# Kernel optimization log

Measured on AMD Instinct MI355X. Metric: run time of the kernel, lower is better.

## Reference

```python
import jax, jax.numpy as jnp
import numpy as np

D_TOK = 64
HID = 128


def _init_linear(key, fan_in, fan_out, bias_fill=None):
    kw, kb = jax.random.split(key)
    bound = 1.0 / np.sqrt(fan_in)
    W = jax.random.uniform(kw, (fan_in, fan_out), jnp.float32, -bound, bound)
    if bias_fill is None:
        b = jax.random.uniform(kb, (fan_out,), jnp.float32, -bound, bound)
    else:
        b = jnp.full((fan_out,), bias_fill, jnp.float32)
    return W, b


def setup_inputs() -> dict:
    key = jax.random.key(0)
    ks = jax.random.split(key, 7)
    N, E = 20000, 16
    tokens = jax.random.normal(ks[0], (N, E, D_TOK), jnp.float32)
    enc_W1, enc_b1 = _init_linear(ks[1], D_TOK, HID)
    enc_W2, enc_b2 = _init_linear(ks[2], HID, HID)
    spec_W1, spec_b1 = _init_linear(ks[3], 4 * HID, HID)
    spec_W2, spec_b2 = _init_linear(ks[4], HID, 1)
    def_W1, def_b1 = _init_linear(ks[5], 3 * HID, HID)
    def_W2, def_b2 = _init_linear(ks[6], HID, 1, bias_fill=-1.0)  # config.defer_bias
    return {
        "tokens": tokens,
        "enc_W1": enc_W1, "enc_b1": enc_b1, "enc_W2": enc_W2, "enc_b2": enc_b2,
        "spec_W1": spec_W1, "spec_b1": spec_b1, "spec_W2": spec_W2, "spec_b2": spec_b2,
        "def_W1": def_W1, "def_b1": def_b1, "def_W2": def_W2, "def_b2": def_b2,
        "full_index": 0,
        "top_k": 2,
    }


def _apply_top_k_mask(logits, full_index, top_k):
    # logits: [N, E]; mimic torch _apply_top_k_mask
    N, E = logits.shape
    if E <= 1:
        return logits
    neg = jnp.finfo(logits.dtype).min
    k = max(1, min(int(top_k), E - 1))
    masked = logits.at[:, full_index].set(neg)
    _, idx = jax.lax.top_k(masked, k)  # [N, k]
    rows = jnp.arange(N)[:, None]
    keep = jnp.zeros((N, E), bool).at[rows, idx].set(True)
    keep = keep.at[:, full_index].set(False)
    return jnp.where(keep, masked, neg)


def reference(tokens, enc_W1, enc_b1, enc_W2, enc_b2,
              spec_W1, spec_b1, spec_W2, spec_b2,
              def_W1, def_b1, def_W2, def_b2,
              full_index, top_k):
    neg = jnp.finfo(tokens.dtype).min
    # token encoder: two Linear+ReLU, applied per (row, expert)
    h = jax.nn.relu(tokens @ enc_W1 + enc_b1)
    encoded = jax.nn.relu(h @ enc_W2 + enc_b2)          # [N, E, H]
    full_token = encoded[:, full_index:full_index + 1]  # [N, 1, H]
    global_token = encoded.mean(axis=1, keepdims=True)  # [N, 1, H]
    token_delta = encoded - full_token
    global_delta = encoded - global_token
    pair = jnp.concatenate([encoded, token_delta, global_delta,
                            jnp.abs(token_delta)], axis=-1)  # [N, E, 4H]
    spec_h = jax.nn.relu(pair @ spec_W1 + spec_b1)
    specialist_logits = (spec_h @ spec_W2 + spec_b2)[..., 0]  # [N, E]
    specialist_logits = specialist_logits.at[:, full_index].set(neg)
    sparse_logits = _apply_top_k_mask(specialist_logits, full_index, top_k)
    w = jax.nn.softmax(sparse_logits, axis=1)
    w = w.at[:, full_index].set(0.0)
    mass = w.sum(axis=1, keepdims=True)
    w = jnp.where(mass > 0, w / jnp.maximum(mass, 1e-8), jnp.zeros_like(w))
    pooled = jnp.concatenate([full_token[:, 0], global_token[:, 0],
                              jnp.abs(token_delta).mean(axis=1)], axis=1)  # [N, 3H]
    def_h = jax.nn.relu(pooled @ def_W1 + def_b1)
    defer_prob = jax.nn.sigmoid(def_h @ def_W2 + def_b2)  # [N, 1]
    return w, defer_prob
```

## Files before the change

### kernel.cpp

```cpp
#include <hip/hip_runtime.h>
#include <math.h>

#define E 16
#define D 64
#define H 128
#define R 4
#define ROWS (R * E)
#define MW 16

__global__ void wabc_prep(const float* __restrict__ specW1, float* __restrict__ wabc) {
    int i = blockIdx.x * blockDim.x + threadIdx.x;
    if (i < H * H) {
        wabc[i] = specW1[i] + specW1[H * H + i] + specW1[2 * H * H + i];
    }
}

template <bool USE_WABC>
__global__ __launch_bounds__(256, 2)
void router_kernel(const float* __restrict__ tokens,
                   const float* __restrict__ encW1, const float* __restrict__ encB1,
                   const float* __restrict__ encW2, const float* __restrict__ encB2,
                   const float* __restrict__ specW1, const float* __restrict__ specB1,
                   const float* __restrict__ specW2,
                   const float* __restrict__ defW1, const float* __restrict__ defB1,
                   const float* __restrict__ defW2, const float* __restrict__ defB2,
                   const int* __restrict__ fiPtr, const int* __restrict__ tkPtr,
                   const float* __restrict__ wabc,
                   float* __restrict__ out, int N) {
    __shared__ float bufA[ROWS * H];
    __shared__ float bufB[ROWS * H];
    __shared__ float s_full[R * H];
    __shared__ float s_glob[R * H];
    __shared__ float s_mabs[R * H];
    __shared__ float s_bias[R * H];
    __shared__ float s_logits[ROWS];
    __shared__ float s_dred[R];

    const int tid   = threadIdx.x;
    const int n0    = blockIdx.x * R;
    const int fi    = fiPtr[0];
    const int lane  = tid & 63;
    const int wq    = tid >> 6;
    const int mbase = wq * MW;
    const int hw    = lane >> 5;
    const int jl    = lane & 31;
    const int jw0   = jl * 4;
    const int mb2   = mbase + hw * 8;

    {
        const size_t base  = (size_t)n0 * (E * D);
        const size_t total = (size_t)N * (E * D);
        float4* dst = (float4*)bufA;
#pragma unroll
        for (int it = 0; it < 4; it++) {
            int f = tid + it * 256;
            size_t off = base + (size_t)f * 4;
            float4 v = make_float4(0.f, 0.f, 0.f, 0.f);
            if (off + 3 < total) v = *(const float4*)(tokens + off);
            dst[f] = v;
        }
    }
    __syncthreads();

    {
        float acc[8][4];
#pragma unroll
        for (int m = 0; m < 8; m++)
#pragma unroll
            for (int j = 0; j < 4; j++) acc[m][j] = 0.f;
#pragma unroll 2
        for (int k = 0; k < D; k += 4) {
            float4 w0 = *(const float4*)(encW1 + (k + 0) * H + jw0);
            float4 w1 = *(const float4*)(encW1 + (k + 1) * H + jw0);
            float4 w2 = *(const float4*)(encW1 + (k + 2) * H + jw0);
            float4 w3 = *(const float4*)(encW1 + (k + 3) * H + jw0);
#pragma unroll
            for (int m = 0; m < 8; m++) {
                float4 t = *(const float4*)(bufA + (mb2 + m) * D + k);
                acc[m][0] = fmaf(t.w, w3.x, fmaf(t.z, w2.x, fmaf(t.y, w1.x, fmaf(t.x, w0.x, acc[m][0]))));
                acc[m][1] = fmaf(t.w, w3.y, fmaf(t.z, w2.y, fmaf(t.y, w1.y, fmaf(t.x, w0.y, acc[m][1]))));
                acc[m][2] = fmaf(t.w, w3.z, fmaf(t.z, w2.z, fmaf(t.y, w1.z, fmaf(t.x, w0.z, acc[m][2]))));
                acc[m][3] = fmaf(t.w, w3.w, fmaf(t.z, w2.w, fmaf(t.y, w1.w, fmaf(t.x, w0.w, acc[m][3]))));
            }
        }
        float4 b = *(const float4*)(encB1 + jw0);
#pragma unroll
        for (int m = 0; m < 8; m++) {
            float4 o;
            o.x = fmaxf(acc[m][0] + b.x, 0.f);
            o.y = fmaxf(acc[m][1] + b.y, 0.f);
            o.z = fmaxf(acc[m][2] + b.z, 0.f);
            o.w = fmaxf(acc[m][3] + b.w, 0.f);
            *(float4*)(bufB + (mb2 + m) * H + jw0) = o;
        }
    }
    __syncthreads();

    {
        float acc[8][4];
#pragma unroll
        for (int m = 0; m < 8; m++)
#pragma unroll
            for (int j = 0; j < 4; j++) acc[m][j] = 0.f;
#pragma unroll 2
        for (int k = 0; k < H; k += 4) {
            float4 w0 = *(const float4*)(encW2 + (k + 0) * H + jw0);
            float4 w1 = *(const float4*)(encW2 + (k + 1) * H + jw0);
            float4 w2 = *(const float4*)(encW2 + (k + 2) * H + jw0);
            float4 w3 = *(const float4*)(encW2 + (k + 3) * H + jw0);
#pragma unroll
            for (int m = 0; m < 8; m++) {
                float4 t = *(const float4*)(bufB + (mb2 + m) * H + k);
                acc[m][0] = fmaf(t.w, w3.x, fmaf(t.z, w2.x, fmaf(t.y, w1.x, fmaf(t.x, w0.x, acc[m][0]))));
                acc[m][1] = fmaf(t.w, w3.y, fmaf(t.z, w2.y, fmaf(t.y, w1.y, fmaf(t.x, w0.y, acc[m][1]))));
                acc[m][2] = fmaf(t.w, w3.z, fmaf(t.z, w2.z, fmaf(t.y, w1.z, fmaf(t.x, w0.z, acc[m][2]))));
                acc[m][3] = fmaf(t.w, w3.w, fmaf(t.z, w2.w, fmaf(t.y, w1.w, fmaf(t.x, w0.w, acc[m][3]))));
            }
        }
        float4 b = *(const float4*)(encB2 + jw0);
#pragma unroll
        for (int m = 0; m < 8; m++) {
            float4 o;
            o.x = fmaxf(acc[m][0] + b.x, 0.f);
            o.y = fmaxf(acc[m][1] + b.y, 0.f);
            o.z = fmaxf(acc[m][2] + b.z, 0.f);
            o.w = fmaxf(acc[m][3] + b.w, 0.f);
            *(float4*)(bufA + (mb2 + m) * H + jw0) = o;
        }
    }
    __syncthreads();

    {
        const int r4 = tid >> 6;
        const int cb = tid & 63;
#pragma unroll
        for (int half = 0; half < 2; half++) {
            const int c = cb + half * 64;
            const float* er = bufA + (r4 * E) * H + c;
            float v[E];
#pragma unroll
            for (int e = 0; e < E; e++) v[e] = er[e * H];
            float s = 0.f;
#pragma unroll
            for (int e = 0; e < E; e++) s += v[e];
            float fc = v[fi];
            float ma = 0.f;
#pragma unroll
            for (int e = 0; e < E; e++) ma += fabsf(v[e] - fc);
            s_full[r4 * H + c] = fc;
            s_glob[r4 * H + c] = s * (1.f / 16.f);
            s_mabs[r4 * H + c] = ma * (1.f / 16.f);
        }
    }
    __syncthreads();

    float* s_pB = bufB;
    float* s_pD = bufB + 2 * R * H;
    {
        const int jp = tid & 63;
        const int jj = jp * 2;
        const int kh = (tid >> 6) & 1;
        const int rg = tid >> 7;
        const int c0 = kh * 64;
        const float* __restrict__ Wb = specW1 + H * H;
        const float* __restrict__ Wc = specW1 + 2 * H * H;
        float accB[2][2] = {{0.f, 0.f}, {0.f, 0.f}};
        float accD[2][2] = {{0.f, 0.f}, {0.f, 0.f}};
        for (int cc = 0; cc < 64; cc++) {
            const int c = c0 + cc;
            float2 wb = *(const float2*)(Wb + c * H + jj);
            float2 wc = *(const float2*)(Wc + c * H + jj);
            float2 d0 = *(const float2*)(defW1 + c * H + jj);
            float2 d1 = *(const float2*)(defW1 + (H + c) * H + jj);
            float2 d2 = *(const float2*)(defW1 + (2 * H + c) * H + jj);
#pragma unroll
            for (int rl = 0; rl < 2; rl++) {
                const int r = rg * 2 + rl;
                float fv = s_full[r * H + c];
                float gv = s_glob[r * H + c];
                float mv = s_mabs[r * H + c];
                accB[rl][0] = fmaf(fv, wb.x, accB[rl][0]);
                accB[rl][1] = fmaf(fv, wb.y, accB[rl][1]);
                accB[rl][0] = fmaf(gv, wc.x, accB[rl][0]);
                accB[rl][1] = fmaf(gv, wc.y, accB[rl][1]);
                accD[rl][0] = fmaf(fv, d0.x, accD[rl][0]);
                accD[rl][1] = fmaf(fv, d0.y, accD[rl][1]);
                accD[rl][0] = fmaf(gv, d1.x, accD[rl][0]);
                accD[rl][1] = fmaf(gv, d1.y, accD[rl][1]);
                accD[rl][0] = fmaf(mv, d2.x, accD[rl][0]);
                accD[rl][1] = fmaf(mv, d2.y, accD[rl][1]);
            }
        }
#pragma unroll
        for (int rl = 0; rl < 2; rl++) {
            const int r = rg * 2 + rl;
            *(float2*)(s_pB + (kh * R + r) * H + jj) = make_float2(accB[rl][0], accB[rl][1]);
            *(float2*)(s_pD + (kh * R + r) * H + jj) = make_float2(accD[rl][0], accD[rl][1]);
        }
    }
    __syncthreads();

    {
        float dv = 0.f;
#pragma unroll
        for (int t = 0; t < 2; t++) {
            const int j = lane + t * 64;
            float pb = s_pB[wq * H + j] + s_pB[(R + wq) * H + j];
            s_bias[wq * H + j] = specB1[j] - pb;
            float pd = defB1[j] + s_pD[wq * H + j] + s_pD[(R + wq) * H + j];
            dv += fmaxf(pd, 0.f) * defW2[j];
        }
#pragma unroll
        for (int off = 32; off; off >>= 1) dv += __shfl_xor(dv, off, 64);
        if (lane == 0) s_dred[wq] = dv;
    }
    __syncthreads();

    {
        float acc[8][4];
#pragma unroll
        for (int m = 0; m < 8; m++)
#pragma unroll
            for (int j = 0; j < 4; j++) acc[m][j] = 0.f;
        const float* __restrict__ Wd = specW1 + 3 * H * H;
        for (int k = 0; k < H; k += 4) {
            float4 wa0, wa1, wa2, wa3;
            if (USE_WABC) {
                wa0 = *(const float4*)(wabc + (k + 0) * H + jw0);
                wa1 = *(const float4*)(wabc + (k + 1) * H + jw0);
                wa2 = *(const float4*)(wabc + (k + 2) * H + jw0);
                wa3 = *(const float4*)(wabc + (k + 3) * H + jw0);
            } else {
#pragma unroll
                for (int t = 0; t < 4; t++) {
                    const float* p = specW1 + (k + t) * H + jw0;
                    float4 x0 = *(const float4*)(p);
                    float4 x1 = *(const float4*)(p + H * H);
                    float4 x2 = *(const float4*)(p + 2 * H * H);
                    float4 s4 = make_float4(x0.x + x1.x + x2.x, x0.y + x1.y + x2.y,
                                            x0.z + x1.z + x2.z, x0.w + x1.w + x2.w);
                    if (t == 0) wa0 = s4; else if (t == 1) wa1 = s4;
                    else if (t == 2) wa2 = s4; else wa3 = s4;
                }
            }
            float4 wd0 = *(const float4*)(Wd + (k + 0) * H + jw0);
            float4 wd1 = *(const float4*)(Wd + (k + 1) * H + jw0);
            float4 wd2 = *(const float4*)(Wd + (k + 2) * H + jw0);
            float4 wd3 = *(const float4*)(Wd + (k + 3) * H + jw0);
            float4 f4 = *(const float4*)(s_full + wq * H + k);
#pragma unroll
            for (int m = 0; m < 8; m++) {
                float4 ev = *(const float4*)(bufA + (mb2 + m) * H + k);
                float ax = fabsf(ev.x - f4.x);
                float ay = fabsf(ev.y - f4.y);
                float az = fabsf(ev.z - f4.z);
                float aw = fabsf(ev.w - f4.w);
#pragma unroll
                for (int j = 0; j < 4; j++) {
                    const float* waj0 = &wa0.x, *waj1 = &wa1.x, *waj2 = &wa2.x, *waj3 = &wa3.x;
                    const float* wdj0 = &wd0.x, *wdj1 = &wd1.x, *wdj2 = &wd2.x, *wdj3 = &wd3.x;
                    float a = acc[m][j];
                    a = fmaf(ev.x, waj0[j], a);
                    a = fmaf(ev.y, waj1[j], a);
                    a = fmaf(ev.z, waj2[j], a);
                    a = fmaf(ev.w, waj3[j], a);
                    a = fmaf(ax, wdj0[j], a);
                    a = fmaf(ay, wdj1[j], a);
                    a = fmaf(az, wdj2[j], a);
                    a = fmaf(aw, wdj3[j], a);
                    acc[m][j] = a;
                }
            }
        }
        float4 bn = *(const float4*)(s_bias + wq * H + jw0);
        float4 w2 = *(const float4*)(specW2 + jw0);
#pragma unroll
        for (int m = 0; m < 8; m++) {
            float p = 0.f;
            p += fmaxf(acc[m][0] + bn.x, 0.f) * w2.x;
            p += fmaxf(acc[m][1] + bn.y, 0.f) * w2.y;
            p += fmaxf(acc[m][2] + bn.z, 0.f) * w2.z;
            p += fmaxf(acc[m][3] + bn.w, 0.f) * w2.w;
#pragma unroll
            for (int off = 1; off < 32; off <<= 1) p += __shfl_xor(p, off, 64);
            if (jl == 0) s_logits[mb2 + m] = p;
        }
    }
    __syncthreads();

    if (tid < R && (n0 + tid) < N) {
        const int r = tid;
        const int n = n0 + r;
        float s = s_dred[r] + defB2[0];
        out[(size_t)N * E + n] = 1.f / (1.f + expf(-s));
        int k = tkPtr[0];
        if (k < 1) k = 1;
        if (k > E - 1) k = E - 1;
        unsigned chosen = 0u;
        for (int kk = 0; kk < k; kk++) {
            float bv = -INFINITY;
            int bi = 0;
            for (int e = 0; e < E; e++) {
                if (e == fi || ((chosen >> e) & 1u)) continue;
                float v = s_logits[r * E + e];
                if (v > bv) { bv = v; bi = e; }
            }
            chosen |= (1u << bi);
        }
        float mx = -INFINITY;
        for (int e = 0; e < E; e++)
            if ((chosen >> e) & 1u) { float v = s_logits[r * E + e]; if (v > mx) mx = v; }
        float ssum = 0.f;
        for (int e = 0; e < E; e++)
            if ((chosen >> e) & 1u) ssum += expf(s_logits[r * E + e] - mx);
        float inv = 1.f / ssum;
        for (int e = 0; e < E; e++) {
            float wv = 0.f;
            if ((chosen >> e) & 1u) wv = expf(s_logits[r * E + e] - mx) * inv;
            out[(size_t)n * E + e] = wv;
        }
    }
}

extern "C" void kernel_launch(void* const* d_in, const int* in_sizes, int n_in,
                              void* d_out, int out_size, void* d_ws, size_t ws_size,
                              hipStream_t stream) {
    (void)n_in; (void)out_size;
    const float* tokens = (const float*)d_in[0];
    const float* encW1  = (const float*)d_in[1];
    const float* encB1  = (const float*)d_in[2];
    const float* encW2  = (const float*)d_in[3];
    const float* encB2  = (const float*)d_in[4];
    const float* specW1 = (const float*)d_in[5];
    const float* specB1 = (const float*)d_in[6];
    const float* specW2 = (const float*)d_in[7];
    const float* defW1  = (const float*)d_in[9];
    const float* defB1  = (const float*)d_in[10];
    const float* defW2  = (const float*)d_in[11];
    const float* defB2  = (const float*)d_in[12];
    const int*   fiPtr  = (const int*)d_in[13];
    const int*   tkPtr  = (const int*)d_in[14];
    float* out = (float*)d_out;

    const int N = in_sizes[0] / (E * D);
    const int grid = (N + R - 1) / R;
    const bool useWs = (d_ws != nullptr) && (ws_size >= (size_t)(H * H * sizeof(float)));

    if (useWs) {
        wabc_prep<<<(H * H + 255) / 256, 256, 0, stream>>>(specW1, (float*)d_ws);
        router_kernel<true><<<grid, 256, 0, stream>>>(
            tokens, encW1, encB1, encW2, encB2, specW1, specB1, specW2,
            defW1, defB1, defW2, defB2, fiPtr, tkPtr, (const float*)d_ws, out, N);
    } else {
        router_kernel<false><<<grid, 256, 0, stream>>>(
            tokens, encW1, encB1, encW2, encB2, specW1, specB1, specW2,
            defW1, defB1, defW2, defB2, fiPtr, tkPtr, nullptr, out, N);
    }
}
```

Baseline: 739.5 us.

## Cut LDS footprint by streaming tokens from global and splitting encoder into halves

Tokens are no longer staged in shared memory; the first encoder layer reads them straight from global memory. The encoder runs in two passes of 32 rows each, so the hidden buffer shrinks to 32 rows, and the pooled/bias scratch arrays are aliased into that buffer. Launch bounds go from 2 to 3 blocks per CU to use the freed LDS and raise occupancy. The cost is more register pressure, an extra barrier pair per pass, and uncoalesced or repeated global token reads.

```diff
diff --git a/kernel.cpp b/kernel.cpp
--- a/kernel.cpp
+++ b/kernel.cpp
@@ -16,7 +16,7 @@
 }
 
 template <bool USE_WABC>
-__global__ __launch_bounds__(256, 2)
+__global__ __launch_bounds__(256, 3)
 void router_kernel(const float* __restrict__ tokens,
                    const float* __restrict__ encW1, const float* __restrict__ encB1,
                    const float* __restrict__ encW2, const float* __restrict__ encB2,
@@ -28,11 +28,7 @@
                    const float* __restrict__ wabc,
                    float* __restrict__ out, int N) {
     __shared__ float bufA[ROWS * H];
-    __shared__ float bufB[ROWS * H];
-    __shared__ float s_full[R * H];
-    __shared__ float s_glob[R * H];
-    __shared__ float s_mabs[R * H];
-    __shared__ float s_bias[R * H];
+    __shared__ float bufB[32 * H];
     __shared__ float s_logits[ROWS];
     __shared__ float s_dred[R];
 
@@ -41,94 +37,93 @@
     const int fi    = fiPtr[0];
     const int lane  = tid & 63;
     const int wq    = tid >> 6;
-    const int mbase = wq * MW;
     const int hw    = lane >> 5;
     const int jl    = lane & 31;
     const int jw0   = jl * 4;
-    const int mb2   = mbase + hw * 8;
-
-    {
-        const size_t base  = (size_t)n0 * (E * D);
-        const size_t total = (size_t)N * (E * D);
-        float4* dst = (float4*)bufA;
-#pragma unroll
-        for (int it = 0; it < 4; it++) {
-            int f = tid + it * 256;
-            size_t off = base + (size_t)f * 4;
-            float4 v = make_float4(0.f, 0.f, 0.f, 0.f);
-            if (off + 3 < total) v = *(const float4*)(tokens + off);
-            dst[f] = v;
-        }
-    }
-    __syncthreads();
-
-    {
-        float acc[8][4];
-#pragma unroll
-        for (int m = 0; m < 8; m++)
-#pragma unroll
-            for (int j = 0; j < 4; j++) acc[m][j] = 0.f;
+
+#pragma unroll 1
+    for (int p = 0; p < 2; p++) {
+        const int lr0 = wq * 8 + hw * 4;
+        const int gr0 = p * 32 + lr0;
+        long rowb = (long)n0 * E + gr0;
+        if (rowb > (long)N * E - 4) rowb = (long)N * E - 4;
+        const float* __restrict__ tb = tokens + rowb * D;
+
+        {
+            float acc[4][4];
+#pragma unroll
+            for (int m = 0; m < 4; m++)
+#pragma unroll
+                for (int j = 0; j < 4; j++) acc[m][j] = 0.f;
 #pragma unroll 2
-        for (int k = 0; k < D; k += 4) {
-            float4 w0 = *(const float4*)(encW1 + (k + 0) * H + jw0);
-            float4 w1 = *(const float4*)(encW1 + (k + 1) * H + jw0);
-            float4 w2 = *(const float4*)(encW1 + (k + 2) * H + jw0);
-            float4 w3 = *(const float4*)(encW1 + (k + 3) * H + jw0);
-#pragma unroll
-            for (int m = 0; m < 8; m++) {
-                float4 t = *(const float4*)(bufA + (mb2 + m) * D + k);
-                acc[m][0] = fmaf(t.w, w3.x, fmaf(t.z, w2.x, fmaf(t.y, w1.x, fmaf(t.x, w0.x, acc[m][0]))));
-                acc[m][1] = fmaf(t.w, w3.y, fmaf(t.z, w2.y, fmaf(t.y, w1.y, fmaf(t.x, w0.y, acc[m][1]))));
-                acc[m][2] = fmaf(t.w, w3.z, fmaf(t.z, w2.z, fmaf(t.y, w1.z, fmaf(t.x, w0.z, acc[m][2]))));
-                acc[m][3] = fmaf(t.w, w3.w, fmaf(t.z, w2.w, fmaf(t.y, w1.w, fmaf(t.x, w0.w, acc[m][3]))));
-            }
-        }
-        float4 b = *(const float4*)(encB1 + jw0);
-#pragma unroll
-        for (int m = 0; m < 8; m++) {
-            float4 o;
-            o.x = fmaxf(acc[m][0] + b.x, 0.f);
-            o.y = fmaxf(acc[m][1] + b.y, 0.f);
-            o.z = fmaxf(acc[m][2] + b.z, 0.f);
-            o.w = fmaxf(acc[m][3] + b.w, 0.f);
-            *(float4*)(bufB + (mb2 + m) * H + jw0) = o;
-        }
-    }
-    __syncthreads();
-
-    {
-        float acc[8][4];
-#pragma unroll
-        for (int m = 0; m < 8; m++)
-#pragma unroll
-            for (int j = 0; j < 4; j++) acc[m][j] = 0.f;
+            for (int k = 0; k < D; k += 4) {
+                float4 w0 = *(const float4*)(encW1 + (k + 0) * H + jw0);
+                float4 w1 = *(const float4*)(encW1 + (k + 1) * H + jw0);
+                float4 w2 = *(const float4*)(encW1 + (k + 2) * H + jw0);
+                float4 w3 = *(const float4*)(encW1 + (k + 3) * H + jw0);
+#pragma unroll
+                for (int m = 0; m < 4; m++) {
+                    float4 t = *(const float4*)(tb + m * D + k);
+                    acc[m][0] = fmaf(t.w, w3.x, fmaf(t.z, w2.x, fmaf(t.y, w1.x, fmaf(t.x, w0.x, acc[m][0]))));
+                    acc[m][1] = fmaf(t.w, w3.y, fmaf(t.z, w2.y, fmaf(t.y, w1.y, fmaf(t.x, w0.y, acc[m][1]))));
+                    acc[m][2] = fmaf(t.w, w3.z, fmaf(t.z, w2.z, fmaf(t.y, w1.z, fmaf(t.x, w0.z, acc[m][2]))));
+                    acc[m][3] = fmaf(t.w, w3.w, fmaf(t.z, w2.w, fmaf(t.y, w1.w, fmaf(t.x, w0.w, acc[m][3]))));
+                }
+            }
+            float4 b = *(const float4*)(encB1 + jw0);
+#pragma unroll
+            for (int m = 0; m < 4; m++) {
+                float4 o;
+                o.x = fmaxf(acc[m][0] + b.x, 0.f);
+                o.y = fmaxf(acc[m][1] + b.y, 0.f);
+                o.z = fmaxf(acc[m][2] + b.z, 0.f);
+                o.w = fmaxf(acc[m][3] + b.w, 0.f);
+                *(float4*)(bufB + (lr0 + m) * H + jw0) = o;
+            }
+        }
+        __syncthreads();
+
+        {
+            float acc[4][4];
+#pragma unroll
+            for (int m = 0; m < 4; m++)
+#pragma unroll
+                for (int j = 0; j < 4; j++) acc[m][j] = 0.f;
 #pragma unroll 2
-        for (int k = 0; k < H; k += 4) {
-            float4 w0 = *(const float4*)(encW2 + (k + 0) * H + jw0);
-            float4 w1 = *(const float4*)(encW2 + (k + 1) * H + jw0);
-            float4 w2 = *(const float4*)(encW2 + (k + 2) * H + jw0);
-            float4 w3 = *(const float4*)(encW2 + (k + 3) * H + jw0);
-#pragma unroll
-            for (int m = 0; m < 8; m++) {
-                float4 t = *(const float4*)(bufB + (mb2 + m) * H + k);
-                acc[m][0] = fmaf(t.w, w3.x, fmaf(t.z, w2.x, fmaf(t.y, w1.x, fmaf(t.x, w0.x, acc[m][0]))));
-                acc[m][1] = fmaf(t.w, w3.y, fmaf(t.z, w2.y, fmaf(t.y, w1.y, fmaf(t.x, w0.y, acc[m][1]))));
-                acc[m][2] = fmaf(t.w, w3.z, fmaf(t.z, w2.z, fmaf(t.y, w1.z, fmaf(t.x, w0.z, acc[m][2]))));
-                acc[m][3] = fmaf(t.w, w3.w, fmaf(t.z, w2.w, fmaf(t.y, w1.w, fmaf(t.x, w0.w, acc[m][3]))));
-            }
-        }
-        float4 b = *(const float4*)(encB2 + jw0);
-#pragma unroll
-        for (int m = 0; m < 8; m++) {
-            float4 o;
-            o.x = fmaxf(acc[m][0] + b.x, 0.f);
-            o.y = fmaxf(acc[m][1] + b.y, 0.f);
-            o.z = fmaxf(acc[m][2] + b.z, 0.f);
-            o.w = fmaxf(acc[m][3] + b.w, 0.f);
-            *(float4*)(bufA + (mb2 + m) * H + jw0) = o;
-        }
-    }
-    __syncthreads();
+            for (int k = 0; k < H; k += 4) {
+                float4 w0 = *(const float4*)(encW2 + (k + 0) * H + jw0);
+                float4 w1 = *(const float4*)(encW2 + (k + 1) * H + jw0);
+                float4 w2 = *(const float4*)(encW2 + (k + 2) * H + jw0);
+                float4 w3 = *(const float4*)(encW2 + (k + 3) * H + jw0);
+#pragma unroll
+                for (int m = 0; m < 4; m++) {
+                    float4 t = *(const float4*)(bufB + (lr0 + m) * H + k);
+                    acc[m][0] = fmaf(t.w, w3.x, fmaf(t.z, w2.x, fmaf(t.y, w1.x, fmaf(t.x, w0.x, acc[m][0]))));
+                    acc[m][1] = fmaf(t.w, w3.y, fmaf(t.z, w2.y, fmaf(t.y, w1.y, fmaf(t.x, w0.y, acc[m][1]))));
+                    acc[m][2] = fmaf(t.w, w3.z, fmaf(t.z, w2.z, fmaf(t.y, w1.z, fmaf(t.x, w0.z, acc[m][2]))));
+                    acc[m][3] = fmaf(t.w, w3.w, fmaf(t.z, w2.w, fmaf(t.y, w1.w, fmaf(t.x, w0.w, acc[m][3]))));
+                }
+            }
+            float4 b = *(const float4*)(encB2 + jw0);
+#pragma unroll
+            for (int m = 0; m < 4; m++) {
+                float4 o;
+                o.x = fmaxf(acc[m][0] + b.x, 0.f);
+                o.y = fmaxf(acc[m][1] + b.y, 0.f);
+                o.z = fmaxf(acc[m][2] + b.z, 0.f);
+                o.w = fmaxf(acc[m][3] + b.w, 0.f);
+                *(float4*)(bufA + (gr0 + m) * H + jw0) = o;
+            }
+        }
+        __syncthreads();
+    }
+
+    float* s_full = bufB;
+    float* s_glob = bufB + 512;
+    float* s_mabs = bufB + 1024;
+    float* s_bias = bufB + 1536;
+    float* s_pB   = bufB + 2048;
+    float* s_pD   = bufB + 3072;
 
     {
         const int r4 = tid >> 6;
@@ -154,8 +149,6 @@
     }
     __syncthreads();
 
-    float* s_pB = bufB;
-    float* s_pD = bufB + 2 * R * H;
     {
         const int jp = tid & 63;
         const int jj = jp * 2;
@@ -217,6 +210,7 @@
     __syncthreads();
 
     {
+        const int mb2 = wq * MW + hw * 8;
         float acc[8][4];
 #pragma unroll
         for (int m = 0; m < 8; m++)
```

Measured after the change: 780.7 us. +5.6%, slower.

## Compute specialist layer with split-bf16 MFMA and exact fp32 fallback near top-k ties

Applied to the files above, without the earlier changes.

Packs the combined specialist weights into three bf16 slices per value in a prep kernel. The main kernel now computes the specialist hidden layer with 16x16x32 bf16 MFMA, using six cross products of the split activations and weights to emulate fp32 accuracy. Rows whose top-k margin falls below a small gap threshold get their logits recomputed exactly in fp32 so the selection matches the reference. It also pads the shared encoded buffer stride to reduce bank conflicts, adds a barrier before the first-layer writeback, and keeps the old fp32 kernel as the no-workspace fallback.

```diff
diff --git a/kernel.cpp b/kernel.cpp
--- a/kernel.cpp
+++ b/kernel.cpp
@@ -7,27 +7,64 @@
 #define R 4
 #define ROWS (R * E)
 #define MW 16
-
-__global__ void wabc_prep(const float* __restrict__ specW1, float* __restrict__ wabc) {
-    int i = blockIdx.x * blockDim.x + threadIdx.x;
-    if (i < H * H) {
-        wabc[i] = specW1[i] + specW1[H * H + i] + specW1[2 * H * H + i];
+#define SA 132
+#define GAP_TAU 2e-3f
+
+typedef __attribute__((ext_vector_type(8))) short bf16x8;
+typedef __attribute__((ext_vector_type(4))) float f32x4;
+
+#define WS_NEED ((size_t)(8 * 8 * 3 * 64 * 8) * sizeof(unsigned short))
+
+__device__ __forceinline__ void split3_8(const float* v, bf16x8& s1, bf16x8& s2, bf16x8& s3) {
+#pragma unroll
+    for (int i = 0; i < 8; i++) {
+        float x = v[i];
+        unsigned u1 = __float_as_uint(x) & 0xffff0000u;
+        float r1 = x - __uint_as_float(u1);
+        unsigned u2 = __float_as_uint(r1) & 0xffff0000u;
+        float r2 = r1 - __uint_as_float(u2);
+        unsigned u3 = __float_as_uint(r2) & 0xffff0000u;
+        s1[i] = (short)(u1 >> 16);
+        s2[i] = (short)(u2 >> 16);
+        s3[i] = (short)(u3 >> 16);
     }
 }
 
-template <bool USE_WABC>
+__global__ void spec_pack(const float* __restrict__ specW1, unsigned short* __restrict__ bw) {
+    int tid = blockIdx.x * blockDim.x + threadIdx.x;
+    if (tid >= 4096) return;
+    const int lane = tid & 63;
+    const int t    = (tid >> 6) & 7;
+    const int s    = tid >> 9;
+    const int n    = t * 16 + (lane & 15);
+    const int kb   = s * 32 + (lane >> 4) * 8;
+    float w[8];
+#pragma unroll
+    for (int j = 0; j < 8; j++) {
+        int k = kb + j;
+        if (k < H) w[j] = specW1[k * H + n] + specW1[(H + k) * H + n] + specW1[(2 * H + k) * H + n];
+        else       w[j] = specW1[(3 * H + (k - H)) * H + n];
+    }
+    bf16x8 s1, s2, s3;
+    split3_8(w, s1, s2, s3);
+    size_t base = ((size_t)(s * 8 + t) * 3) * 512 + (size_t)lane * 8;
+    *(bf16x8*)(bw + base)        = s1;
+    *(bf16x8*)(bw + base + 512)  = s2;
+    *(bf16x8*)(bw + base + 1024) = s3;
+}
+
 __global__ __launch_bounds__(256, 2)
-void router_kernel(const float* __restrict__ tokens,
-                   const float* __restrict__ encW1, const float* __restrict__ encB1,
-                   const float* __restrict__ encW2, const float* __restrict__ encB2,
-                   const float* __restrict__ specW1, const float* __restrict__ specB1,
-                   const float* __restrict__ specW2,
-                   const float* __restrict__ defW1, const float* __restrict__ defB1,
-                   const float* __restrict__ defW2, const float* __restrict__ defB2,
-                   const int* __restrict__ fiPtr, const int* __restrict__ tkPtr,
-                   const float* __restrict__ wabc,
-                   float* __restrict__ out, int N) {
-    __shared__ float bufA[ROWS * H];
+void router_mfma(const float* __restrict__ tokens,
+                 const float* __restrict__ encW1, const float* __restrict__ encB1,
+                 const float* __restrict__ encW2, const float* __restrict__ encB2,
+                 const float* __restrict__ specW1, const float* __restrict__ specB1,
+                 const float* __restrict__ specW2,
+                 const float* __restrict__ defW1, const float* __restrict__ defB1,
+                 const float* __restrict__ defW2, const float* __restrict__ defB2,
+                 const int* __restrict__ fiPtr, const int* __restrict__ tkPtr,
+                 const unsigned short* __restrict__ bslices,
+                 float* __restrict__ out, int N) {
+    __shared__ float bufA[ROWS * SA];
     __shared__ float bufB[ROWS * H];
     __shared__ float s_full[R * H];
     __shared__ float s_glob[R * H];
@@ -35,6 +72,7 @@
     __shared__ float s_bias[R * H];
     __shared__ float s_logits[ROWS];
     __shared__ float s_dred[R];
+    __shared__ int   s_flag[R];
 
     const int tid   = threadIdx.x;
     const int n0    = blockIdx.x * R;
@@ -84,6 +122,7 @@
             }
         }
         float4 b = *(const float4*)(encB1 + jw0);
+        __syncthreads();
 #pragma unroll
         for (int m = 0; m < 8; m++) {
             float4 o;
@@ -125,7 +164,7 @@
             o.y = fmaxf(acc[m][1] + b.y, 0.f);
             o.z = fmaxf(acc[m][2] + b.z, 0.f);
             o.w = fmaxf(acc[m][3] + b.w, 0.f);
-            *(float4*)(bufA + (mb2 + m) * H + jw0) = o;
+            *(float4*)(bufA + (mb2 + m) * SA + jw0) = o;
         }
     }
     __syncthreads();
@@ -136,10 +175,10 @@
 #pragma unroll
         for (int half = 0; half < 2; half++) {
             const int c = cb + half * 64;
-            const float* er = bufA + (r4 * E) * H + c;
+            const float* er = bufA + (r4 * E) * SA + c;
             float v[E];
 #pragma unroll
-            for (int e = 0; e < E; e++) v[e] = er[e * H];
+            for (int e = 0; e < E; e++) v[e] = er[e * SA];
             float s = 0.f;
 #pragma unroll
             for (int e = 0; e < E; e++) s += v[e];
@@ -217,6 +256,365 @@
     __syncthreads();
 
     {
+        const int m    = lane & 15;
+        const int quad = lane >> 4;
+        const int row  = mbase + m;
+        f32x4 acc[8];
+#pragma unroll
+        for (int t = 0; t < 8; t++)
+#pragma unroll
+            for (int g = 0; g < 4; g++) acc[t][g] = 0.f;
+#pragma unroll 1
+        for (int s = 0; s < 8; s++) {
+            const int kb = s * 32 + quad * 8;
+            float v[8];
+            if (kb < H) {
+                float4 a0 = *(const float4*)(bufA + row * SA + kb);
+                float4 a1 = *(const float4*)(bufA + row * SA + kb + 4);
+                v[0] = a0.x; v[1] = a0.y; v[2] = a0.z; v[3] = a0.w;
+                v[4] = a1.x; v[5] = a1.y; v[6] = a1.z; v[7] = a1.w;
+            } else {
+                const int kc = kb - H;
+                float4 a0 = *(const float4*)(bufA + row * SA + kc);
+                float4 a1 = *(const float4*)(bufA + row * SA + kc + 4);
+                float4 f0 = *(const float4*)(s_full + wq * H + kc);
+                float4 f1 = *(const float4*)(s_full + wq * H + kc + 4);
+                v[0] = fabsf(a0.x - f0.x); v[1] = fabsf(a0.y - f0.y);
+                v[2] = fabsf(a0.z - f0.z); v[3] = fabsf(a0.w - f0.w);
+                v[4] = fabsf(a1.x - f1.x); v[5] = fabsf(a1.y - f1.y);
+                v[6] = fabsf(a1.z - f1.z); v[7] = fabsf(a1.w - f1.w);
+            }
+            bf16x8 x1, x2, x3;
+            split3_8(v, x1, x2, x3);
+#pragma unroll
+            for (int t = 0; t < 8; t++) {
+                const unsigned short* bp = bslices + ((size_t)(s * 8 + t) * 3) * 512 + (size_t)lane * 8;
+                bf16x8 b1 = *(const bf16x8*)(bp);
+                bf16x8 b2 = *(const bf16x8*)(bp + 512);
+                bf16x8 b3 = *(const bf16x8*)(bp + 1024);
+                acc[t] = __builtin_amdgcn_mfma_f32_16x16x32_bf16(x1, b1, acc[t], 0, 0, 0);
+                acc[t] = __builtin_amdgcn_mfma_f32_16x16x32_bf16(x1, b2, acc[t], 0, 0, 0);
+                acc[t] = __builtin_amdgcn_mfma_f32_16x16x32_bf16(x2, b1, acc[t], 0, 0, 0);
+                acc[t] = __builtin_amdgcn_mfma_f32_16x16x32_bf16(x1, b3, acc[t], 0, 0, 0);
+                acc[t] = __builtin_amdgcn_mfma_f32_16x16x32_bf16(x3, b1, acc[t], 0, 0, 0);
+                acc[t] = __builtin_amdgcn_mfma_f32_16x16x32_bf16(x2, b2, acc[t], 0, 0, 0);
+            }
+        }
+        float part[4] = {0.f, 0.f, 0.f, 0.f};
+#pragma unroll
+        for (int t = 0; t < 8; t++) {
+            const int j = t * 16 + m;
+            float bj = s_bias[wq * H + j];
+            float wj = specW2[j];
+#pragma unroll
+            for (int g = 0; g < 4; g++)
+                part[g] += fmaxf(acc[t][g] + bj, 0.f) * wj;
+        }
+#pragma unroll
+        for (int off = 1; off < 16; off <<= 1)
+#pragma unroll
+            for (int g = 0; g < 4; g++) part[g] += __shfl_xor(part[g], off, 64);
+        if (m == 0)
+#pragma unroll
+            for (int g = 0; g < 4; g++) s_logits[wq * E + quad * 4 + g] = part[g];
+    }
+    __syncthreads();
+
+    if (tid < R) {
+        int k = tkPtr[0];
+        if (k < 1) k = 1;
+        if (k > E - 1) k = E - 1;
+        float lg[E];
+#pragma unroll
+        for (int e = 0; e < E; e++) lg[e] = s_logits[tid * E + e];
+        unsigned chosen = 0u;
+        for (int kk = 0; kk < k; kk++) {
+            float bv = -INFINITY; int bi = 0;
+            for (int e = 0; e < E; e++) {
+                if (e == fi || ((chosen >> e) & 1u)) continue;
+                if (lg[e] > bv) { bv = lg[e]; bi = e; }
+            }
+            chosen |= (1u << bi);
+        }
+        float cmin = INFINITY, umax = -INFINITY;
+        for (int e = 0; e < E; e++) {
+            if (e == fi) continue;
+            if ((chosen >> e) & 1u) cmin = fminf(cmin, lg[e]);
+            else                    umax = fmaxf(umax, lg[e]);
+        }
+        s_flag[tid] = (cmin - umax < GAP_TAU) ? 1 : 0;
+    }
+    __syncthreads();
+
+    for (int r = 0; r < R; r++) {
+        if (s_flag[r]) {
+            const int e  = tid >> 4;
+            const int jb = (tid & 15) * 8;
+            const float* er = bufA + (r * E + e) * SA;
+            const float* fr = s_full + r * H;
+            float a[8];
+#pragma unroll
+            for (int jj = 0; jj < 8; jj++) a[jj] = s_bias[r * H + jb + jj];
+            for (int kk = 0; kk < H; kk++) {
+                float ev = er[kk];
+                float ad = fabsf(ev - fr[kk]);
+                const float* p = specW1 + kk * H + jb;
+                float4 w0a = *(const float4*)(p);
+                float4 w0b = *(const float4*)(p + 4);
+                float4 w1a = *(const float4*)(p + H * H);
+                float4 w1b = *(const float4*)(p + H * H + 4);
+                float4 w2a = *(const float4*)(p + 2 * H * H);
+                float4 w2b = *(const float4*)(p + 2 * H * H + 4);
+                float4 w3a = *(const float4*)(p + 3 * H * H);
+                float4 w3b = *(const float4*)(p + 3 * H * H + 4);
+                a[0] = fmaf(ad, w3a.x, fmaf(ev, w0a.x + w1a.x + w2a.x, a[0]));
+                a[1] = fmaf(ad, w3a.y, fmaf(ev, w0a.y + w1a.y + w2a.y, a[1]));
+                a[2] = fmaf(ad, w3a.z, fmaf(ev, w0a.z + w1a.z + w2a.z, a[2]));
+                a[3] = fmaf(ad, w3a.w, fmaf(ev, w0a.w + w1a.w + w2a.w, a[3]));
+                a[4] = fmaf(ad, w3b.x, fmaf(ev, w0b.x + w1b.x + w2b.x, a[4]));
+                a[5] = fmaf(ad, w3b.y, fmaf(ev, w0b.y + w1b.y + w2b.y, a[5]));
+                a[6] = fmaf(ad, w3b.z, fmaf(ev, w0b.z + w1b.z + w2b.z, a[6]));
+                a[7] = fmaf(ad, w3b.w, fmaf(ev, w0b.w + w1b.w + w2b.w, a[7]));
+            }
+            float part = 0.f;
+#pragma unroll
+            for (int jj = 0; jj < 8; jj++)
+                part += fmaxf(a[jj], 0.f) * specW2[jb + jj];
+#pragma unroll
+            for (int off = 1; off < 16; off <<= 1) part += __shfl_xor(part, off, 64);
+            if ((tid & 15) == 0) s_logits[r * E + e] = part;
+        }
+    }
+    __syncthreads();
+
+    if (tid < R && (n0 + tid) < N) {
+        const int r = tid;
+        const int n = n0 + r;
+        float s = s_dred[r] + defB2[0];
+        out[(size_t)N * E + n] = 1.f / (1.f + expf(-s));
+        int k = tkPtr[0];
+        if (k < 1) k = 1;
+        if (k > E - 1) k = E - 1;
+        unsigned chosen = 0u;
+        for (int kk = 0; kk < k; kk++) {
+            float bv = -INFINITY; int bi = 0;
+            for (int e = 0; e < E; e++) {
+                if (e == fi || ((chosen >> e) & 1u)) continue;
+                float v = s_logits[r * E + e];
+                if (v > bv) { bv = v; bi = e; }
+            }
+            chosen |= (1u << bi);
+        }
+        float mx = -INFINITY;
+        for (int e = 0; e < E; e++)
+            if ((chosen >> e) & 1u) { float v = s_logits[r * E + e]; if (v > mx) mx = v; }
+        float ssum = 0.f;
+        for (int e = 0; e < E; e++)
+            if ((chosen >> e) & 1u) ssum += expf(s_logits[r * E + e] - mx);
+        float inv = 1.f / ssum;
+        for (int e = 0; e < E; e++) {
+            float wv = 0.f;
+            if ((chosen >> e) & 1u) wv = expf(s_logits[r * E + e] - mx) * inv;
+            out[(size_t)n * E + e] = wv;
+        }
+    }
+}
+
+__global__ __launch_bounds__(256, 2)
+void router_fp32(const float* __restrict__ tokens,
+                 const float* __restrict__ encW1, const float* __restrict__ encB1,
+                 const float* __restrict__ encW2, const float* __restrict__ encB2,
+                 const float* __restrict__ specW1, const float* __restrict__ specB1,
+                 const float* __restrict__ specW2,
+                 const float* __restrict__ defW1, const float* __restrict__ defB1,
+                 const float* __restrict__ defW2, const float* __restrict__ defB2,
+                 const int* __restrict__ fiPtr, const int* __restrict__ tkPtr,
+                 float* __restrict__ out, int N) {
+    __shared__ float bufA[ROWS * H];
+    __shared__ float bufB[ROWS * H];
+    __shared__ float s_full[R * H];
+    __shared__ float s_glob[R * H];
+    __shared__ float s_mabs[R * H];
+    __shared__ float s_bias[R * H];
+    __shared__ float s_logits[ROWS];
+    __shared__ float s_dred[R];
+
+    const int tid   = threadIdx.x;
+    const int n0    = blockIdx.x * R;
+    const int fi    = fiPtr[0];
+    const int lane  = tid & 63;
+    const int wq    = tid >> 6;
+    const int mbase = wq * MW;
+    const int hw    = lane >> 5;
+    const int jl    = lane & 31;
+    const int jw0   = jl * 4;
+    const int mb2   = mbase + hw * 8;
+
+    {
+        const size_t base  = (size_t)n0 * (E * D);
+        const size_t total = (size_t)N * (E * D);
+        float4* dst = (float4*)bufA;
+#pragma unroll
+        for (int it = 0; it < 4; it++) {
+            int f = tid + it * 256;
+            size_t off = base + (size_t)f * 4;
+            float4 v = make_float4(0.f, 0.f, 0.f, 0.f);
+            if (off + 3 < total) v = *(const float4*)(tokens + off);
+            dst[f] = v;
+        }
+    }
+    __syncthreads();
+    {
+        float acc[8][4];
+#pragma unroll
+        for (int m = 0; m < 8; m++)
+#pragma unroll
+            for (int j = 0; j < 4; j++) acc[m][j] = 0.f;
+#pragma unroll 2
+        for (int k = 0; k < D; k += 4) {
+            float4 w0 = *(const float4*)(encW1 + (k + 0) * H + jw0);
+            float4 w1 = *(const float4*)(encW1 + (k + 1) * H + jw0);
+            float4 w2 = *(const float4*)(encW1 + (k + 2) * H + jw0);
+            float4 w3 = *(const float4*)(encW1 + (k + 3) * H + jw0);
+#pragma unroll
+            for (int m = 0; m < 8; m++) {
+                float4 t = *(const float4*)(bufA + (mb2 + m) * D + k);
+                acc[m][0] = fmaf(t.w, w3.x, fmaf(t.z, w2.x, fmaf(t.y, w1.x, fmaf(t.x, w0.x, acc[m][0]))));
+                acc[m][1] = fmaf(t.w, w3.y, fmaf(t.z, w2.y, fmaf(t.y, w1.y, fmaf(t.x, w0.y, acc[m][1]))));
+                acc[m][2] = fmaf(t.w, w3.z, fmaf(t.z, w2.z, fmaf(t.y, w1.z, fmaf(t.x, w0.z, acc[m][2]))));
+                acc[m][3] = fmaf(t.w, w3.w, fmaf(t.z, w2.w, fmaf(t.y, w1.w, fmaf(t.x, w0.w, acc[m][3]))));
+            }
+        }
+        float4 b = *(const float4*)(encB1 + jw0);
+        __syncthreads();
+#pragma unroll
+        for (int m = 0; m < 8; m++) {
+            float4 o;
+            o.x = fmaxf(acc[m][0] + b.x, 0.f);
+            o.y = fmaxf(acc[m][1] + b.y, 0.f);
+            o.z = fmaxf(acc[m][2] + b.z, 0.f);
+            o.w = fmaxf(acc[m][3] + b.w, 0.f);
+            *(float4*)(bufB + (mb2 + m) * H + jw0) = o;
+        }
+    }
+    __syncthreads();
+    {
+        float acc[8][4];
+#pragma unroll
+        for (int m = 0; m < 8; m++)
+#pragma unroll
+            for (int j = 0; j < 4; j++) acc[m][j] = 0.f;
+#pragma unroll 2
+        for (int k = 0; k < H; k += 4) {
+            float4 w0 = *(const float4*)(encW2 + (k + 0) * H + jw0);
+            float4 w1 = *(const float4*)(encW2 + (k + 1) * H + jw0);
+            float4 w2 = *(const float4*)(encW2 + (k + 2) * H + jw0);
+            float4 w3 = *(const float4*)(encW2 + (k + 3) * H + jw0);
+#pragma unroll
+            for (int m = 0; m < 8; m++) {
+                float4 t = *(const float4*)(bufB + (mb2 + m) * H + k);
+                acc[m][0] = fmaf(t.w, w3.x, fmaf(t.z, w2.x, fmaf(t.y, w1.x, fmaf(t.x, w0.x, acc[m][0]))));
+                acc[m][1] = fmaf(t.w, w3.y, fmaf(t.z, w2.y, fmaf(t.y, w1.y, fmaf(t.x, w0.y, acc[m][1]))));
+                acc[m][2] = fmaf(t.w, w3.z, fmaf(t.z, w2.z, fmaf(t.y, w1.z, fmaf(t.x, w0.z, acc[m][2]))));
+                acc[m][3] = fmaf(t.w, w3.w, fmaf(t.z, w2.w, fmaf(t.y, w1.w, fmaf(t.x, w0.w, acc[m][3]))));
+            }
+        }
+        float4 b = *(const float4*)(encB2 + jw0);
+#pragma unroll
+        for (int m = 0; m < 8; m++) {
+            float4 o;
+            o.x = fmaxf(acc[m][0] + b.x, 0.f);
+            o.y = fmaxf(acc[m][1] + b.y, 0.f);
+            o.z = fmaxf(acc[m][2] + b.z, 0.f);
+            o.w = fmaxf(acc[m][3] + b.w, 0.f);
+            *(float4*)(bufA + (mb2 + m) * H + jw0) = o;
+        }
+    }
+    __syncthreads();
+    {
+        const int r4 = tid >> 6;
+        const int cb = tid & 63;
+#pragma unroll
+        for (int half = 0; half < 2; half++) {
+            const int c = cb + half * 64;
+            const float* er = bufA + (r4 * E) * H + c;
+            float v[E];
+#pragma unroll
+            for (int e = 0; e < E; e++) v[e] = er[e * H];
+            float s = 0.f;
+#pragma unroll
+            for (int e = 0; e < E; e++) s += v[e];
+            float fc = v[fi];
+            float ma = 0.f;
+#pragma unroll
+            for (int e = 0; e < E; e++) ma += fabsf(v[e] - fc);
+            s_full[r4 * H + c] = fc;
+            s_glob[r4 * H + c] = s * (1.f / 16.f);
+            s_mabs[r4 * H + c] = ma * (1.f / 16.f);
+        }
+    }
+    __syncthreads();
+    float* s_pB = bufB;
+    float* s_pD = bufB + 2 * R * H;
+    {
+        const int jp = tid & 63;
+        const int jj = jp * 2;
+        const int kh = (tid >> 6) & 1;
+        const int rg = tid >> 7;
+        const int c0 = kh * 64;
+        const float* __restrict__ Wb = specW1 + H * H;
+        const float* __restrict__ Wc = specW1 + 2 * H * H;
+        float accB[2][2] = {{0.f, 0.f}, {0.f, 0.f}};
+        float accD[2][2] = {{0.f, 0.f}, {0.f, 0.f}};
+        for (int cc = 0; cc < 64; cc++) {
+            const int c = c0 + cc;
+            float2 wb = *(const float2*)(Wb + c * H + jj);
+            float2 wc = *(const float2*)(Wc + c * H + jj);
+            float2 d0 = *(const float2*)(defW1 + c * H + jj);
+            float2 d1 = *(const float2*)(defW1 + (H + c) * H + jj);
+            float2 d2 = *(const float2*)(defW1 + (2 * H + c) * H + jj);
+#pragma unroll
+            for (int rl = 0; rl < 2; rl++) {
+                const int r = rg * 2 + rl;
+                float fv = s_full[r * H + c];
+                float gv = s_glob[r * H + c];
+                float mv = s_mabs[r * H + c];
+                accB[rl][0] = fmaf(fv, wb.x, accB[rl][0]);
+                accB[rl][1] = fmaf(fv, wb.y, accB[rl][1]);
+                accB[rl][0] = fmaf(gv, wc.x, accB[rl][0]);
+                accB[rl][1] = fmaf(gv, wc.y, accB[rl][1]);
+                accD[rl][0] = fmaf(fv, d0.x, accD[rl][0]);
+                accD[rl][1] = fmaf(fv, d0.y, accD[rl][1]);
+                accD[rl][0] = fmaf(gv, d1.x, accD[rl][0]);
+                accD[rl][1] = fmaf(gv, d1.y, accD[rl][1]);
+                accD[rl][0] = fmaf(mv, d2.x, accD[rl][0]);
+                accD[rl][1] = fmaf(mv, d2.y, accD[rl][1]);
+            }
+        }
+#pragma unroll
+        for (int rl = 0; rl < 2; rl++) {
+            const int r = rg * 2 + rl;
+            *(float2*)(s_pB + (kh * R + r) * H + jj) = make_float2(accB[rl][0], accB[rl][1]);
+            *(float2*)(s_pD + (kh * R + r) * H + jj) = make_float2(accD[rl][0], accD[rl][1]);
+        }
+    }
+    __syncthreads();
+    {
+        float dv = 0.f;
+#pragma unroll
+        for (int t = 0; t < 2; t++) {
+            const int j = lane + t * 64;
+            float pb = s_pB[wq * H + j] + s_pB[(R + wq) * H + j];
+            s_bias[wq * H + j] = specB1[j] - pb;
+            float pd = defB1[j] + s_pD[wq * H + j] + s_pD[(R + wq) * H + j];
+            dv += fmaxf(pd, 0.f) * defW2[j];
+        }
+#pragma unroll
+        for (int off = 32; off; off >>= 1) dv += __shfl_xor(dv, off, 64);
+        if (lane == 0) s_dred[wq] = dv;
+    }
+    __syncthreads();
+    {
         float acc[8][4];
 #pragma unroll
         for (int m = 0; m < 8; m++)
@@ -225,23 +623,16 @@
         const float* __restrict__ Wd = specW1 + 3 * H * H;
         for (int k = 0; k < H; k += 4) {
             float4 wa0, wa1, wa2, wa3;
-            if (USE_WABC) {
-                wa0 = *(const float4*)(wabc + (k + 0) * H + jw0);
-                wa1 = *(const float4*)(wabc + (k + 1) * H + jw0);
-                wa2 = *(const float4*)(wabc + (k + 2) * H + jw0);
-                wa3 = *(const float4*)(wabc + (k + 3) * H + jw0);
-            } else {
-#pragma unroll
-                for (int t = 0; t < 4; t++) {
-                    const float* p = specW1 + (k + t) * H + jw0;
-                    float4 x0 = *(const float4*)(p);
-                    float4 x1 = *(const float4*)(p + H * H);
-                    float4 x2 = *(const float4*)(p + 2 * H * H);
-                    float4 s4 = make_float4(x0.x + x1.x + x2.x, x0.y + x1.y + x2.y,
-                                            x0.z + x1.z + x2.z, x0.w + x1.w + x2.w);
-                    if (t == 0) wa0 = s4; else if (t == 1) wa1 = s4;
-                    else if (t == 2) wa2 = s4; else wa3 = s4;
-                }
+#pragma unroll
+            for (int t = 0; t < 4; t++) {
+                const float* p = specW1 + (k + t) * H + jw0;
+                float4 x0 = *(const float4*)(p);
+                float4 x1 = *(const float4*)(p + H * H);
+                float4 x2 = *(const float4*)(p + 2 * H * H);
+                float4 s4 = make_float4(x0.x + x1.x + x2.x, x0.y + x1.y + x2.y,
+                                        x0.z + x1.z + x2.z, x0.w + x1.w + x2.w);
+                if (t == 0) wa0 = s4; else if (t == 1) wa1 = s4;
+                else if (t == 2) wa2 = s4; else wa3 = s4;
             }
             float4 wd0 = *(const float4*)(Wd + (k + 0) * H + jw0);
             float4 wd1 = *(const float4*)(Wd + (k + 1) * H + jw0);
@@ -287,7 +678,6 @@
         }
     }
     __syncthreads();
-
     if (tid < R && (n0 + tid) < N) {
         const int r = tid;
         const int n = n0 + r;
@@ -298,8 +688,7 @@
         if (k > E - 1) k = E - 1;
         unsigned chosen = 0u;
         for (int kk = 0; kk < k; kk++) {
-            float bv = -INFINITY;
-            int bi = 0;
+            float bv = -INFINITY; int bi = 0;
             for (int e = 0; e < E; e++) {
                 if (e == fi || ((chosen >> e) & 1u)) continue;
                 float v = s_logits[r * E + e];
@@ -344,16 +733,16 @@
 
     const int N = in_sizes[0] / (E * D);
     const int grid = (N + R - 1) / R;
-    const bool useWs = (d_ws != nullptr) && (ws_size >= (size_t)(H * H * sizeof(float)));
-
-    if (useWs) {
-        wabc_prep<<<(H * H + 255) / 256, 256, 0, stream>>>(specW1, (float*)d_ws);
-        router_kernel<true><<<grid, 256, 0, stream>>>(
+
+    if (d_ws != nullptr && ws_size >= WS_NEED) {
+        spec_pack<<<16, 256, 0, stream>>>(specW1, (unsigned short*)d_ws);
+        router_mfma<<<grid, 256, 0, stream>>>(
             tokens, encW1, encB1, encW2, encB2, specW1, specB1, specW2,
-            defW1, defB1, defW2, defB2, fiPtr, tkPtr, (const float*)d_ws, out, N);
+            defW1, defB1, defW2, defB2, fiPtr, tkPtr,
+            (const unsigned short*)d_ws, out, N);
     } else {
-        router_kernel<false><<<grid, 256, 0, stream>>>(
+        router_fp32<<<grid, 256, 0, stream>>>(
             tokens, encW1, encB1, encW2, encB2, specW1, specB1, specW2,
-            defW1, defB1, defW2, defB2, fiPtr, tkPtr, nullptr, out, N);
+            defW1, defB1, defW2, defB2, fiPtr, tkPtr, out, N);
     }
 }
```

Result: slower. 1.273 ms (+72.2%).
